# Performance work log

Measured on AMD Instinct MI355X. Metric: run time of the kernel, lower is better.

The kernel has to match this reference:

```python
import jax, jax.numpy as jnp
import numpy as np

T, B, INPUT_DIM, HIDDEN = 512, 1024, 64, 8  # n_qubits == hidden_dim in the torch module


def _linear_init(k, fan_in, fan_out):
    k1, k2 = jax.random.split(k)
    bound = 1.0 / np.sqrt(fan_in)
    W = jax.random.uniform(k1, (fan_in, fan_out), minval=-bound, maxval=bound, dtype=jnp.float32)
    b = jax.random.uniform(k2, (fan_out,), minval=-bound, maxval=bound, dtype=jnp.float32)
    return W, b


def setup_inputs() -> dict:
    key = jax.random.key(0)
    ks = jax.random.split(key, 12)
    inp = {"inputs": jax.random.normal(ks[0], (T, B, INPUT_DIM), dtype=jnp.float32)}
    names = ["f", "i", "u", "o"]
    for j, n in enumerate(names):
        W, b = _linear_init(ks[1 + j], INPUT_DIM + HIDDEN, HIDDEN)
        inp["W" + n], inp["b" + n] = W, b
        # trainable RX angles of each QLayer (torchquantum inits uniform in [0, 2pi))
        inp["th_" + n] = jax.random.uniform(ks[5 + j], (HIDDEN,), minval=0.0, maxval=2.0 * np.pi, dtype=jnp.float32)
    inp["Wh2k"], inp["bh2k"] = _linear_init(ks[9], HIDDEN, HIDDEN)
    inp["Wi2k"], inp["bi2k"] = _linear_init(ks[10], INPUT_DIM, HIDDEN)
    return inp


def _qlayer(pre, theta):
    # QLayer: |0..0> -> RX(pre_i) RX(theta_i) on wire i (same-wire RX angles add),
    # then CNOT ring (0->1, 1->2, ..., n-1->0), then <Z_w> per wire.
    # Product-state probs per qubit: E[(-1)^{b_i}] = cos(a_i). The CNOT chain maps
    # bit w (w>=1) to XOR(b_0..b_w) and bit 0 to XOR(b_1..b_{n-1}); independence gives
    # <Z_w> = prod_{i<=w} cos(a_i) (w>=1) and <Z_0> = prod_{i>=1} cos(a_i). Exact.
    z = jnp.cos(pre + theta)                              # [B, n]
    cp = jnp.cumprod(z, axis=1)
    z0 = jnp.prod(z[:, 1:], axis=1, keepdims=True)
    return jnp.concatenate([z0, cp[:, 1:]], axis=1)       # [B, n]


def _kernel(kx, ky):
    # KernalAnsatz: RY(x_i) then RY(-y_i) per wire == RY(x_i - y_i); amplitude of
    # |0..0> is prod_i cos((x_i - y_i)/2); Kernel returns its abs. Exact closed form.
    return jnp.abs(jnp.prod(jnp.cos(0.5 * (kx - ky)), axis=1, keepdims=True))  # [B, 1]


def reference(inputs, Wf, bf, Wi, bi, Wu, bu, Wo, bo, th_f, th_i, th_u, th_o, Wh2k, bh2k, Wi2k, bi2k):
    Bsz = inputs.shape[1]
    h0 = jnp.zeros((Bsz, HIDDEN), dtype=inputs.dtype)
    c0 = jnp.zeros((Bsz, HIDDEN), dtype=inputs.dtype)

    def step(carry, x):
        hx, cx = carry
        comb = jnp.concatenate([x, hx], axis=1)                       # [B, D+H]
        w = _kernel(hx @ Wh2k + bh2k, x @ Wi2k + bi2k)                # [B, 1] -> broadcast
        f = jax.nn.sigmoid(_qlayer(comb @ Wf + bf, th_f) * w)
        i = jax.nn.sigmoid(_qlayer(comb @ Wi + bi, th_i) * w)
        g = jnp.tanh(_qlayer(comb @ Wu + bu, th_u) * w)
        o = jax.nn.sigmoid(_qlayer(comb @ Wo + bo, th_o) * w)
        cx = f * cx + i * g
        hx = o * jnp.tanh(cx)
        return (hx, cx), hx

    (hx, cx), outputs = jax.lax.scan(step, (h0, c0), inputs)
    return outputs, hx, cx
```

## Files before the change

kernel.cpp:

```cpp
#include <hip/hip_runtime.h>

#define TT 512
#define BB 1024
#define INV2PI 0.15915494309189535f
#define INV4PI 0.07957747154594767f

typedef __attribute__((ext_vector_type(2))) float f2;

__device__ __forceinline__ float frcp(float x){ return __builtin_amdgcn_rcpf(x); }
__device__ __forceinline__ float fcosrev(float r){
  return __builtin_amdgcn_cosf(__builtin_amdgcn_fractf(r));
}

#define DPPR(v, ctrl) __int_as_float(__builtin_amdgcn_update_dpp(__float_as_int(v), __float_as_int(v), (ctrl), 0xF, 0xF, false))
#define DPP1(v, ctrl) __int_as_float(__builtin_amdgcn_update_dpp(0x3f800000, __float_as_int(v), (ctrl), 0xF, 0xF, false))


__global__ __launch_bounds__(256,1) void qlstm_prep(
    const float* __restrict__ Wf, const float* __restrict__ Wi,
    const float* __restrict__ Wu, const float* __restrict__ Wo,
    const float* __restrict__ Wi2k,
    float* __restrict__ gw)
{
  int idx = blockIdx.x*256 + threadIdx.x;
  if (idx >= 64*40) return;
  int d = idx / 40, cc = idx - d*40;
  float v;
  if (cc < 32){
    int pi = cc >> 1, slot = cc & 1;
    int jj = pi >> 1, pbc = pi & 1;
    int g = 2*pbc + slot;
    const float* W = (g==0)?Wf:((g==1)?Wi:((g==2)?Wu:Wo));
    v = W[d*8+jj] * INV2PI;
  } else {
    v = Wi2k[d*8 + (cc-32)] * INV4PI;
  }
  gw[idx] = v;
}

__global__ __launch_bounds__(256,1) void qlstm_fused(
    const float* __restrict__ x,
    const float* __restrict__ gw,
    const float* __restrict__ Wf, const float* __restrict__ bfp, const float* __restrict__ thf,
    const float* __restrict__ Wi, const float* __restrict__ bip, const float* __restrict__ thi,
    const float* __restrict__ Wu, const float* __restrict__ bup, const float* __restrict__ thu,
    const float* __restrict__ Wo, const float* __restrict__ bop, const float* __restrict__ tho,
    const float* __restrict__ Wh2k, const float* __restrict__ bh2k,
    const float* __restrict__ Wi2k, const float* __restrict__ bi2k,
    float* __restrict__ out)
{
  __shared__ float bias[40];
  __shared__ float xp[3][32][4][40];

  int tid = threadIdx.x;
  int b0 = blockIdx.x * 4;

  if (tid < 40){
    int cc = tid; float v;
    if (cc < 32){
      int pi = cc >> 1, slot = cc & 1;
      int jj = pi >> 1, pbc = pi & 1;
      int g = 2*pbc + slot;
      const float* bp = (g==0)?bfp:((g==1)?bip:((g==2)?bup:bop));
      const float* tp = (g==0)?thf:((g==1)?thi:((g==2)?thu:tho));
      v = (bp[jj] + tp[jj]) * INV2PI;
    } else {
      v = (bi2k[cc-32] - bh2k[cc-32]) * INV4PI;
    }
    bias[cc] = v;
  }

  int wid = tid >> 6;
  bool pb = (tid & 1) != 0;
  int j  = (tid >> 1) & 7;
  int bl = (tid >> 4) & 3;

  int plane = tid - 64;
  int ptl = plane >> 2, pbl = plane & 3;

  auto produce = [&](int ck){
    int t = ck*32 + ptl;
    const float4* xr = (const float4*)(x + ((size_t)t*BB + b0 + pbl)*64);
    float4 acc[10];
    const float4* b4 = (const float4*)bias;
#pragma unroll
    for (int q=0;q<10;++q) acc[q] = b4[q];
#pragma unroll 1
    for (int k4=0;k4<16;++k4){
      float4 xv = xr[k4];
#pragma unroll
      for (int dd=0; dd<4; ++dd){
        float s = (dd==0)?xv.x:((dd==1)?xv.y:((dd==2)?xv.z:xv.w));
        const float4* w4 = (const float4*)&gw[(k4*4+dd)*40];
#pragma unroll
        for (int q=0;q<10;++q){
          acc[q].x += s*w4[q].x; acc[q].y += s*w4[q].y;
          acc[q].z += s*w4[q].z; acc[q].w += s*w4[q].w;
        }
      }
    }
    float4* dst = (float4*)&xp[ck%3][ptl][pbl][0];
#pragma unroll
    for (int q=0;q<10;++q) dst[q] = acc[q];
  };

  const float* WA = pb ? Wu : Wf;
  const float* WB = pb ? Wo : Wi;
  float wsc[24];
#pragma unroll
  for (int s=0;s<8;++s){
    int k = (j + s) & 7;
    wsc[s]    = WA[(64+k)*8 + j] * INV2PI;
    wsc[8+s]  = WB[(64+k)*8 + j] * INV2PI;
    wsc[16+s] = Wh2k[k*8 + j] * INV4PI;
  }
  f2 wA01={wsc[0],wsc[1]},  wA23={wsc[2],wsc[3]},  wA45={wsc[4],wsc[5]},  wA67={wsc[6],wsc[7]};
  f2 wB01={wsc[8],wsc[9]},  wB23={wsc[10],wsc[11]},wB45={wsc[12],wsc[13]},wB67={wsc[14],wsc[15]};
  f2 wK01={wsc[16],wsc[17]},wK23={wsc[18],wsc[19]},wK45={wsc[20],wsc[21]},wK67={wsc[22],wsc[23]};

  float preA = pb ? 1.0f : 0.5f;
  f2 postMP= { pb ? 1.0f : 0.5f, 0.5f };
  f2 postBP= { pb ? 0.0f : 0.5f, 0.5f };
  const f2 C6 = {0.00359213f,0.00359213f};
  const f2 C5 = {-0.00886324f,-0.00886324f};
  const f2 C4 = {0.02186948f,0.02186948f};
  const f2 C3 = {-0.05396825f,-0.05396825f};
  const f2 C2 = {0.13333333f,0.13333333f};
  const f2 C1 = {-0.33333333f,-0.33333333f};
  const f2 C0 = {1.0f,1.0f};

  float h = 0.f, c = 0.f;

  __syncthreads();

  if (wid == 1 || wid == 2){
    produce(0);
    produce(1);
  }

  __syncthreads();

  int oAB = bl*40 + 2*(tid & 15);
  int oK  = bl*40 + 32 + j;
  f2 xABq[4]; float xKq[4];
  int osto = (b0 + bl)*8 + j;

  if (wid == 0){
#pragma unroll
    for (int i=0;i<4;++i){
      const float* sp = &xp[0][i][0][0];
      xABq[i] = *(const f2*)&sp[oAB];
      xKq[i]  = sp[oK];
    }
  }

  auto STEP = [&](const float* __restrict__ pp, int u){
    float xA = xABq[u].x, xB = xABq[u].y, xK = xKq[u];
    xABq[u] = *(const f2*)&pp[oAB];
    xKq[u]  = pp[oK];

    float hr1 = DPPR(h,0x12E), hr2 = DPPR(h,0x12C), hr3 = DPPR(h,0x12A),
          hr4 = DPPR(h,0x128), hr5 = DPPR(h,0x126), hr6 = DPPR(h,0x124),
          hr7 = DPPR(h,0x122);
    f2 hp0 = {h, hr1}, hp1 = {hr2, hr3}, hp2 = {hr4, hr5}, hp3 = {hr6, hr7};

    f2 accA = hp0*wA01; accA = hp1*wA23 + accA; accA = hp2*wA45 + accA; accA = hp3*wA67 + accA;
    f2 accB = hp0*wB01; accB = hp1*wB23 + accB; accB = hp2*wB45 + accB; accB = hp3*wB67 + accB;
    f2 accK = hp0*wK01; accK = hp1*wK23 + accK; accK = hp2*wK45 + accK; accK = hp3*wK67 + accK;
    float aA = accA.x + accA.y;
    float aB = accB.x + accB.y;
    float aK = accK.x + accK.y;

    float kv = fcosrev(aK - xK);
    kv *= DPPR(kv,0x12E);
    kv *= DPPR(kv,0x12C);
    kv *= DPPR(kv,0x128);
    float wk = fabsf(kv);
    float wkA = wk * preA;
    float wkB = wk * 0.5f;

#define CUMQ(ZV, WKX, GQ) { \
    float zz = (ZV); \
    float pz = zz; \
    pz *= DPP1(pz,0x112); \
    pz *= DPP1(pz,0x114); \
    pz *= DPP1(pz,0x118); \
    float q = (j==0)? 1.0f : zz; \
    q *= DPPR(q,0x12E); \
    q *= DPPR(q,0x12C); \
    q *= DPPR(q,0x128); \
    GQ = ((j==0)? q : pz) * (WKX); }

    float yA, yB;
    CUMQ(fcosrev(aA + xA), wkA, yA)
    CUMQ(fcosrev(aB + xB), wkB, yB)
#undef CUMQ

    f2 y = {yA, yB};
    f2 s2 = y * y;
    f2 p = s2*C6 + C5;
    p = p*s2 + C4;
    p = p*s2 + C3;
    p = p*s2 + C2;
    p = p*s2 + C1;
    p = p*s2 + C0;
    f2 t2 = y * p;
    f2 act = t2*postMP + postBP;
    float actA = act.x, actB = act.y;

    float gAo = DPPR(actA,0xB1);
    float gBo = DPPR(actB,0xB1);
    float fv = pb ? gAo  : actA;
    float uv = pb ? actA : gAo;
    float iv = pb ? gBo  : actB;
    float ov = pb ? actB : gBo;

    c = fmaf(fv, c, iv*uv);
    float c2 = c * c;
    float num = fmaf(c2, c2 + 105.0f, 945.0f);
    float den = fmaf(c2, fmaf(c2, 15.0f, 420.0f), 945.0f);
    float tch = c * num * frcp(den);
    h = ov * tch;

    out[osto] = h;
    osto += BB*8;
  };

  for (int k = 0; k < 16; ++k){
    if (wid == 0){
      const float* baseA = &xp[k%3][0][0][0];
      const float* baseB = &xp[(k+1)%3][0][0][0];
#pragma unroll 1
      for (int s4 = 0; s4 < 28; s4 += 4){
        const float* bp4 = baseA + (s4+4)*160;
#pragma unroll
        for (int u = 0; u < 4; ++u) STEP(bp4 + u*160, u);
      }
#pragma unroll
      for (int u = 0; u < 4; ++u) STEP(baseB + u*160, u);
    } else if (wid == 1 || wid == 2){
      if (k + 2 < 16) produce(k + 2);
    }
    __syncthreads();
  }

  if (wid == 0){
    out[(size_t)TT*BB*8 + (size_t)(b0+bl)*8 + j] = h;
    out[(size_t)TT*BB*8 + (size_t)BB*8 + (size_t)(b0+bl)*8 + j] = c;
  }
}

extern "C" void kernel_launch(void* const* d_in, const int* in_sizes, int n_in,
                              void* d_out, int out_size, void* d_ws, size_t ws_size,
                              hipStream_t stream)
{
  const float* x    = (const float*)d_in[0];
  const float* Wf   = (const float*)d_in[1];
  const float* bf   = (const float*)d_in[2];
  const float* thf  = (const float*)d_in[3];
  const float* Wi   = (const float*)d_in[4];
  const float* bi   = (const float*)d_in[5];
  const float* thi  = (const float*)d_in[6];
  const float* Wu   = (const float*)d_in[7];
  const float* bu   = (const float*)d_in[8];
  const float* thu  = (const float*)d_in[9];
  const float* Wo   = (const float*)d_in[10];
  const float* bo   = (const float*)d_in[11];
  const float* tho  = (const float*)d_in[12];
  const float* Wh2k = (const float*)d_in[13];
  const float* bh2k = (const float*)d_in[14];
  const float* Wi2k = (const float*)d_in[15];
  const float* bi2k = (const float*)d_in[16];
  float* out = (float*)d_out;
  float* gw  = (float*)d_ws;
  (void)ws_size; (void)in_sizes; (void)n_in; (void)out_size;

  qlstm_prep<<<10, 256, 0, stream>>>(Wf, Wi, Wu, Wo, Wi2k, gw);
  qlstm_fused<<<BB/4, 256, 0, stream>>>(
      x, gw, Wf,bf,thf, Wi,bi,thi, Wu,bu,thu, Wo,bo,tho,
      Wh2k, bh2k, Wi2k, bi2k, out);
}
```

Measured before the change: 153.7 us.

## Split recurrent scan across two wavefronts with one gate per lane

Result: faster. 150.1 us (-2.3%).

```diff
diff --git a/kernel.cpp b/kernel.cpp
--- a/kernel.cpp
+++ b/kernel.cpp
@@ -5,7 +5,7 @@
 #define INV2PI 0.15915494309189535f
 #define INV4PI 0.07957747154594767f
 
-typedef __attribute__((ext_vector_type(2))) float f2;
+typedef __attribute__((ext_vector_type(2))) unsigned u2v;
 
 __device__ __forceinline__ float frcp(float x){ return __builtin_amdgcn_rcpf(x); }
 __device__ __forceinline__ float fcosrev(float r){
@@ -27,9 +27,7 @@
   int d = idx / 40, cc = idx - d*40;
   float v;
   if (cc < 32){
-    int pi = cc >> 1, slot = cc & 1;
-    int jj = pi >> 1, pbc = pi & 1;
-    int g = 2*pbc + slot;
+    int jj = cc >> 2, g = cc & 3;
     const float* W = (g==0)?Wf:((g==1)?Wi:((g==2)?Wu:Wo));
     v = W[d*8+jj] * INV2PI;
   } else {
@@ -58,9 +56,7 @@
   if (tid < 40){
     int cc = tid; float v;
     if (cc < 32){
-      int pi = cc >> 1, slot = cc & 1;
-      int jj = pi >> 1, pbc = pi & 1;
-      int g = 2*pbc + slot;
+      int jj = cc >> 2, g = cc & 3;
       const float* bp = (g==0)?bfp:((g==1)?bip:((g==2)?bup:bop));
       const float* tp = (g==0)?thf:((g==1)?thi:((g==2)?thu:tho));
       v = (bp[jj] + tp[jj]) * INV2PI;
@@ -71,9 +67,14 @@
   }
 
   int wid = tid >> 6;
-  bool pb = (tid & 1) != 0;
-  int j  = (tid >> 1) & 7;
-  int bl = (tid >> 4) & 3;
+  int L  = tid & 63;
+  int gl = L & 1;
+  int j  = (L >> 1) & 7;
+  int el = (L >> 4) & 1;
+  bool hi = L >= 32;
+  int g  = (hi ? 2 : 0) + gl;
+  int elb = ((wid == 3) ? 2 : 0) + el;
+  bool isScan = (wid == 0) || (wid == 3);
 
   int plane = tid - 64;
   int ptl = plane >> 2, pbl = plane & 3;
@@ -104,30 +105,17 @@
     for (int q=0;q<10;++q) dst[q] = acc[q];
   };
 
-  const float* WA = pb ? Wu : Wf;
-  const float* WB = pb ? Wo : Wi;
-  float wsc[24];
+  const float* Wg = (g==0)?Wf:((g==1)?Wi:((g==2)?Wu:Wo));
+  float wG[8], wK[8];
 #pragma unroll
   for (int s=0;s<8;++s){
     int k = (j + s) & 7;
-    wsc[s]    = WA[(64+k)*8 + j] * INV2PI;
-    wsc[8+s]  = WB[(64+k)*8 + j] * INV2PI;
-    wsc[16+s] = Wh2k[k*8 + j] * INV4PI;
-  }
-  f2 wA01={wsc[0],wsc[1]},  wA23={wsc[2],wsc[3]},  wA45={wsc[4],wsc[5]},  wA67={wsc[6],wsc[7]};
-  f2 wB01={wsc[8],wsc[9]},  wB23={wsc[10],wsc[11]},wB45={wsc[12],wsc[13]},wB67={wsc[14],wsc[15]};
-  f2 wK01={wsc[16],wsc[17]},wK23={wsc[18],wsc[19]},wK45={wsc[20],wsc[21]},wK67={wsc[22],wsc[23]};
-
-  float preA = pb ? 1.0f : 0.5f;
-  f2 postMP= { pb ? 1.0f : 0.5f, 0.5f };
-  f2 postBP= { pb ? 0.0f : 0.5f, 0.5f };
-  const f2 C6 = {0.00359213f,0.00359213f};
-  const f2 C5 = {-0.00886324f,-0.00886324f};
-  const f2 C4 = {0.02186948f,0.02186948f};
-  const f2 C3 = {-0.05396825f,-0.05396825f};
-  const f2 C2 = {0.13333333f,0.13333333f};
-  const f2 C1 = {-0.33333333f,-0.33333333f};
-  const f2 C0 = {1.0f,1.0f};
+    wG[s] = Wg[(64+k)*8 + j] * INV2PI;
+    wK[s] = Wh2k[k*8 + j] * INV4PI;
+  }
+  float preG  = (g==2) ? 1.0f : 0.5f;
+  float postM = (g==2) ? 1.0f : 0.5f;
+  float postB = (g==2) ? 0.0f : 0.5f;
 
   float h = 0.f, c = 0.f;
 
@@ -140,80 +128,80 @@
 
   __syncthreads();
 
-  int oAB = bl*40 + 2*(tid & 15);
-  int oK  = bl*40 + 32 + j;
-  f2 xABq[4]; float xKq[4];
-  int osto = (b0 + bl)*8 + j;
-
-  if (wid == 0){
+  int oG = elb*40 + 4*j + g;
+  int oK = elb*40 + 32 + j;
+  float xGq[4], xKq[4];
+  int osto = (b0 + elb)*8 + j;
+
+  if (isScan){
+#pragma unroll
+    for (int i=0;i<4;++i){
+      const float* sp = &xp[0][i>>2][0][0];
+      (void)sp;
+    }
 #pragma unroll
     for (int i=0;i<4;++i){
       const float* sp = &xp[0][i][0][0];
-      xABq[i] = *(const f2*)&sp[oAB];
-      xKq[i]  = sp[oK];
+      xGq[i] = sp[oG];
+      xKq[i] = sp[oK];
     }
   }
 
   auto STEP = [&](const float* __restrict__ pp, int u){
-    float xA = xABq[u].x, xB = xABq[u].y, xK = xKq[u];
-    xABq[u] = *(const f2*)&pp[oAB];
-    xKq[u]  = pp[oK];
+    float xG = xGq[u], xK = xKq[u];
+    xGq[u] = pp[oG];
+    xKq[u] = pp[oK];
 
     float hr1 = DPPR(h,0x12E), hr2 = DPPR(h,0x12C), hr3 = DPPR(h,0x12A),
           hr4 = DPPR(h,0x128), hr5 = DPPR(h,0x126), hr6 = DPPR(h,0x124),
           hr7 = DPPR(h,0x122);
-    f2 hp0 = {h, hr1}, hp1 = {hr2, hr3}, hp2 = {hr4, hr5}, hp3 = {hr6, hr7};
-
-    f2 accA = hp0*wA01; accA = hp1*wA23 + accA; accA = hp2*wA45 + accA; accA = hp3*wA67 + accA;
-    f2 accB = hp0*wB01; accB = hp1*wB23 + accB; accB = hp2*wB45 + accB; accB = hp3*wB67 + accB;
-    f2 accK = hp0*wK01; accK = hp1*wK23 + accK; accK = hp2*wK45 + accK; accK = hp3*wK67 + accK;
-    float aA = accA.x + accA.y;
-    float aB = accB.x + accB.y;
-    float aK = accK.x + accK.y;
+
+    float aG =        h*wG[0];
+    aG = fmaf(hr1,wG[1],aG); aG = fmaf(hr2,wG[2],aG); aG = fmaf(hr3,wG[3],aG);
+    aG = fmaf(hr4,wG[4],aG); aG = fmaf(hr5,wG[5],aG); aG = fmaf(hr6,wG[6],aG);
+    aG = fmaf(hr7,wG[7],aG);
+    float aK =        h*wK[0];
+    aK = fmaf(hr1,wK[1],aK); aK = fmaf(hr2,wK[2],aK); aK = fmaf(hr3,wK[3],aK);
+    aK = fmaf(hr4,wK[4],aK); aK = fmaf(hr5,wK[5],aK); aK = fmaf(hr6,wK[6],aK);
+    aK = fmaf(hr7,wK[7],aK);
 
     float kv = fcosrev(aK - xK);
     kv *= DPPR(kv,0x12E);
     kv *= DPPR(kv,0x12C);
     kv *= DPPR(kv,0x128);
-    float wk = fabsf(kv);
-    float wkA = wk * preA;
-    float wkB = wk * 0.5f;
-
-#define CUMQ(ZV, WKX, GQ) { \
-    float zz = (ZV); \
-    float pz = zz; \
-    pz *= DPP1(pz,0x112); \
-    pz *= DPP1(pz,0x114); \
-    pz *= DPP1(pz,0x118); \
-    float q = (j==0)? 1.0f : zz; \
-    q *= DPPR(q,0x12E); \
-    q *= DPPR(q,0x12C); \
-    q *= DPPR(q,0x128); \
-    GQ = ((j==0)? q : pz) * (WKX); }
-
-    float yA, yB;
-    CUMQ(fcosrev(aA + xA), wkA, yA)
-    CUMQ(fcosrev(aB + xB), wkB, yB)
-#undef CUMQ
-
-    f2 y = {yA, yB};
-    f2 s2 = y * y;
-    f2 p = s2*C6 + C5;
-    p = p*s2 + C4;
-    p = p*s2 + C3;
-    p = p*s2 + C2;
-    p = p*s2 + C1;
-    p = p*s2 + C0;
-    f2 t2 = y * p;
-    f2 act = t2*postMP + postBP;
-    float actA = act.x, actB = act.y;
-
-    float gAo = DPPR(actA,0xB1);
-    float gBo = DPPR(actB,0xB1);
-    float fv = pb ? gAo  : actA;
-    float uv = pb ? actA : gAo;
-    float iv = pb ? gBo  : actB;
-    float ov = pb ? actB : gBo;
+    float wkG = fabsf(kv) * preG;
+
+    float zz = fcosrev(aG + xG);
+    float pz = zz;
+    pz *= DPP1(pz,0x112);
+    pz *= DPP1(pz,0x114);
+    pz *= DPP1(pz,0x118);
+    float q = (j==0) ? 1.0f : zz;
+    q *= DPPR(q,0x12E);
+    q *= DPPR(q,0x12C);
+    q *= DPPR(q,0x128);
+    float y = ((j==0) ? q : pz) * wkG;
+
+    float s2 = y*y;
+    float p = fmaf(s2, 0.00359213f, -0.00886324f);
+    p = fmaf(p, s2, 0.02186948f);
+    p = fmaf(p, s2, -0.05396825f);
+    p = fmaf(p, s2, 0.13333333f);
+    p = fmaf(p, s2, -0.33333333f);
+    p = fmaf(p, s2, 1.0f);
+    float act = fmaf(y*p, postM, postB);
+
+    float actX1 = DPPR(act, 0xB1);
+    float p1 = gl ? actX1 : act;
+    float p2 = gl ? act : actX1;
+    u2v r1 = __builtin_amdgcn_permlane32_swap(__float_as_uint(p1), __float_as_uint(p1), false, false);
+    u2v r2 = __builtin_amdgcn_permlane32_swap(__float_as_uint(p2), __float_as_uint(p2), false, false);
+    float b0v = __uint_as_float(hi ? r1.x : r1.y);
+    float b1v = __uint_as_float(hi ? r2.x : r2.y);
+    float fv = hi ? b0v : p1;
+    float iv = hi ? b1v : p2;
+    float uv = hi ? p1 : b0v;
+    float ov = hi ? p2 : b1v;
 
     c = fmaf(fv, c, iv*uv);
     float c2 = c * c;
@@ -227,7 +215,7 @@
   };
 
   for (int k = 0; k < 16; ++k){
-    if (wid == 0){
+    if (isScan){
       const float* baseA = &xp[k%3][0][0][0];
       const float* baseB = &xp[(k+1)%3][0][0][0];
 #pragma unroll 1
@@ -238,15 +226,15 @@
       }
 #pragma unroll
       for (int u = 0; u < 4; ++u) STEP(baseB + u*160, u);
-    } else if (wid == 1 || wid == 2){
+    } else {
       if (k + 2 < 16) produce(k + 2);
     }
     __syncthreads();
   }
 
-  if (wid == 0){
-    out[(size_t)TT*BB*8 + (size_t)(b0+bl)*8 + j] = h;
-    out[(size_t)TT*BB*8 + (size_t)BB*8 + (size_t)(b0+bl)*8 + j] = c;
+  if (isScan){
+    out[(size_t)TT*BB*8 + (size_t)(b0+elb)*8 + j] = h;
+    out[(size_t)TT*BB*8 + (size_t)BB*8 + (size_t)(b0+elb)*8 + j] = c;
   }
 }
 
```
